# Performance work log

Hardware: AMD Instinct MI355X
Metric: run time of the kernel (lower is better)

## Reference

```python
import jax, jax.numpy as jnp
import numpy as np

N = 10000        # total_num
BS = 100         # batch_size (BatchNorm is applied per micro-batch in train mode)
IN_CH = 3
D = 128          # out_channels
TOPK = 50
BN_EPS = 1e-5


def setup_inputs() -> dict:
    key = jax.random.key(0)
    k1, k2, k3, k4 = jax.random.split(key, 4)
    feat = 32 * 32 * IN_CH
    inputs = jax.random.normal(k1, (N, IN_CH, 32, 32), dtype=jnp.float32)
    # nn.Linear(32*32*in_channels, out_channels)
    W1 = jax.random.normal(k2, (D, feat), dtype=jnp.float32) / np.sqrt(feat)
    b1 = jnp.zeros((D,), jnp.float32)
    # BatchNorm1d(out_channels) affine params
    gamma = jnp.ones((D,), jnp.float32)
    beta = jnp.zeros((D,), jnp.float32)
    # nn.Linear(out_channels, 1) -> weight [1, D] stored as vector, scalar bias
    sw = jax.random.normal(k3, (D,), dtype=jnp.float32) / np.sqrt(D)
    sb = jax.random.normal(k4, (), dtype=jnp.float32) * 0.01
    return {"inputs": inputs, "W1": W1, "b1": b1, "gamma": gamma,
            "beta": beta, "sw": sw, "sb": sb}


def _forward(inputs, W1, b1, gamma, beta, sw, sb):
    n = inputs.shape[0]
    # self.main is identity (undefined backbone); flatten + linear
    x = inputs.reshape(n, -1) @ W1.T + b1                      # [N, D]
    # BatchNorm1d in train mode, applied per batch of BS rows (as in the loop)
    xb = x.reshape(n // BS, BS, D)
    mean = xb.mean(axis=1, keepdims=True)
    var = xb.var(axis=1, keepdims=True)                        # biased, like torch BN
    outputs = ((xb - mean) * jax.lax.rsqrt(var + BN_EPS) * gamma + beta).reshape(n, D)
    # score[i,j] = ReLU( sum_k sw[k]*(x_i[k]-x_j[k])^2 + sb )
    a = (outputs * outputs) @ sw                               # [N]
    cross = (outputs * sw) @ outputs.T                         # [N, N]
    scores = jax.nn.relu(a[:, None] + a[None, :] - 2.0 * cross + sb)
    vals, idx = jax.lax.top_k(scores, TOPK)                    # [N, TOPK]
    vals = jax.nn.softmax(vals, axis=-1)
    S = jnp.zeros((n, n), outputs.dtype).at[jnp.arange(n)[:, None], idx].set(vals)
    return outputs, S


def reference(inputs, W1, b1, gamma, beta, sw, sb):
    return _forward(inputs, W1, b1, gamma, beta, sw, sb)
```

## Files before the change

kernel.cpp:

```cpp
#include <hip/hip_runtime.h>
#include <cstdint>

#define N_TOTAL 10000
#define D 128
#define FEAT 3072
#define BS_BN 100
#define TOPK 50

typedef unsigned int uint;
typedef short short8 __attribute__((ext_vector_type(8)));
typedef float f32x4 __attribute__((ext_vector_type(4)));
union U16 { uint4 u; short8 b; };

__device__ inline void split8(float4 f0, float4 f1, U16& h, U16& l) {
  float f[8] = {f0.x, f0.y, f0.z, f0.w, f1.x, f1.y, f1.z, f1.w};
  uint hb[8], lb[8];
#pragma unroll
  for (int e = 0; e < 8; ++e) {
    uint b = __float_as_uint(f[e]);
    uint hx = b & 0xFFFF0000u;
    float lf = f[e] - __uint_as_float(hx);
    hb[e] = b >> 16;
    lb[e] = __float_as_uint(lf) >> 16;
  }
  h.u = make_uint4(hb[0] | (hb[1] << 16), hb[2] | (hb[3] << 16),
                   hb[4] | (hb[5] << 16), hb[6] | (hb[7] << 16));
  l.u = make_uint4(lb[0] | (lb[1] << 16), lb[2] | (lb[3] << 16),
                   lb[4] | (lb[5] << 16), lb[6] | (lb[7] << 16));
}

__global__ __launch_bounds__(256) void k_gemm1(const float* __restrict__ in,
                                               const float* __restrict__ W1,
                                               float* __restrict__ x) {
  __shared__ alignas(16) float Af[128 * 44];
  __shared__ alignas(16) float Bf[128 * 44];
  const int t = threadIdx.x;
  const int lane = t & 63, wid = t >> 6;
  const int q = lane >> 4, l15 = lane & 15;
  const int i0 = blockIdx.x * 128;
  const int k0 = blockIdx.y * 768;
  const int wm = (wid & 1) * 64, wn = (wid >> 1) * 64;

  f32x4 acc[4][4];
#pragma unroll
  for (int mt = 0; mt < 4; ++mt)
#pragma unroll
    for (int nt = 0; nt < 4; ++nt) acc[mt][nt] = (f32x4){0.f, 0.f, 0.f, 0.f};

  for (int kb = k0; kb < k0 + 768; kb += 32) {
    __syncthreads();
#pragma unroll
    for (int s = 0; s < 4; ++s) {
      int idx = t + 256 * s;
      int row = idx >> 3, f4 = (idx & 7) * 4;
      int gi = i0 + row; if (gi > N_TOTAL - 1) gi = N_TOTAL - 1;
      *(float4*)&Af[row * 44 + f4] = *(const float4*)&in[(size_t)gi * FEAT + kb + f4];
      *(float4*)&Bf[row * 44 + f4] = *(const float4*)&W1[(size_t)row * FEAT + kb + f4];
    }
    __syncthreads();
    U16 Ah[4], Al[4], Bh[4], Bl[4];
#pragma unroll
    for (int mt = 0; mt < 4; ++mt) {
      int ro = (wm + mt * 16 + l15) * 44 + q * 8;
      float4 x0 = *(const float4*)&Af[ro];
      float4 x1 = *(const float4*)&Af[ro + 4];
      split8(x0, x1, Ah[mt], Al[mt]);
    }
#pragma unroll
    for (int nt = 0; nt < 4; ++nt) {
      int ro = (wn + nt * 16 + l15) * 44 + q * 8;
      float4 x0 = *(const float4*)&Bf[ro];
      float4 x1 = *(const float4*)&Bf[ro + 4];
      split8(x0, x1, Bh[nt], Bl[nt]);
    }
#pragma unroll
    for (int mt = 0; mt < 4; ++mt)
#pragma unroll
      for (int nt = 0; nt < 4; ++nt) {
        acc[mt][nt] = __builtin_amdgcn_mfma_f32_16x16x32_bf16(Ah[mt].b, Bh[nt].b, acc[mt][nt], 0, 0, 0);
        acc[mt][nt] = __builtin_amdgcn_mfma_f32_16x16x32_bf16(Ah[mt].b, Bl[nt].b, acc[mt][nt], 0, 0, 0);
        acc[mt][nt] = __builtin_amdgcn_mfma_f32_16x16x32_bf16(Al[mt].b, Bh[nt].b, acc[mt][nt], 0, 0, 0);
      }
  }

#pragma unroll
  for (int mt = 0; mt < 4; ++mt) {
#pragma unroll
    for (int r = 0; r < 4; ++r) {
      int gi = i0 + wm + mt * 16 + q * 4 + r;
      if (gi >= N_TOTAL) continue;
#pragma unroll
      for (int nt = 0; nt < 4; ++nt)
        atomicAdd(&x[(size_t)gi * D + wn + nt * 16 + l15], acc[mt][nt][r]);
    }
  }
}

__global__ __launch_bounds__(128) void k_bn(const float* __restrict__ x,
                                            const float* __restrict__ b1,
                                            const float* __restrict__ gamma,
                                            const float* __restrict__ beta,
                                            const float* __restrict__ sw,
                                            float* __restrict__ out_final,
                                            float* __restrict__ outf,
                                            float* __restrict__ wsw) {
  const int b = blockIdx.x, c = threadIdx.x;
  const float bias = b1[c];
  float s = 0.f, s2 = 0.f;
  const float* xp = x + (size_t)b * BS_BN * D + c;
  for (int r = 0; r < BS_BN; ++r) {
    float v = xp[(size_t)r * D] + bias;
    s += v; s2 = fmaf(v, v, s2);
  }
  float mean = s * (1.f / BS_BN);
  float var = s2 * (1.f / BS_BN) - mean * mean;
  float scale = gamma[c] * rsqrtf(var + 1e-5f);
  float shift = beta[c] - mean * scale;
  float swc = sw[c];
  float* op  = out_final + (size_t)b * BS_BN * D + c;
  float* ofp = outf + (size_t)b * BS_BN * D + c;
  float* wp  = wsw + (size_t)b * BS_BN * D + c;
  for (int r = 0; r < BS_BN; ++r) {
    float v = fmaf(xp[(size_t)r * D] + bias, scale, shift);
    op[(size_t)r * D] = v;
    ofp[(size_t)r * D] = v;
    wp[(size_t)r * D] = v * swc;
  }
}

__global__ __launch_bounds__(256) void k_arow(const float* __restrict__ outf,
                                              const float* __restrict__ sw,
                                              float* __restrict__ aarr) {
  const int t = threadIdx.x;
  const int lane = t & 63;
  const int row = blockIdx.x * 4 + (t >> 6);
  float o1 = outf[(size_t)row * D + lane];
  float o2 = outf[(size_t)row * D + 64 + lane];
  float v = sw[lane] * o1 * o1 + sw[64 + lane] * o2 * o2;
#pragma unroll
  for (int off = 32; off >= 1; off >>= 1) v += __shfl_xor(v, off);
  if (lane == 0) aarr[row] = v;
}

__global__ __launch_bounds__(256) void k_score(const float* __restrict__ outf,
                                               const float* __restrict__ wsw,
                                               const float* __restrict__ aarr,
                                               const float* __restrict__ sbp,
                                               float* __restrict__ S) {
  __shared__ alignas(16) float Af[128 * 44];
  __shared__ alignas(16) float Bf[128 * 44];
  const int t = threadIdx.x;
  const int lane = t & 63, wid = t >> 6;
  const int q = lane >> 4, l15 = lane & 15;
  const int ib = blockIdx.x * 128, jb = blockIdx.y * 128;
  const int wm = (wid & 1) * 64, wn = (wid >> 1) * 64;

  f32x4 acc[4][4];
#pragma unroll
  for (int mt = 0; mt < 4; ++mt)
#pragma unroll
    for (int nt = 0; nt < 4; ++nt) acc[mt][nt] = (f32x4){0.f, 0.f, 0.f, 0.f};

  for (int kb = 0; kb < D; kb += 32) {
    __syncthreads();
#pragma unroll
    for (int s = 0; s < 4; ++s) {
      int idx = t + 256 * s;
      int row = idx >> 3, f4 = (idx & 7) * 4;
      int gi = ib + row; if (gi > N_TOTAL - 1) gi = N_TOTAL - 1;
      int gj = jb + row; if (gj > N_TOTAL - 1) gj = N_TOTAL - 1;
      *(float4*)&Af[row * 44 + f4] = *(const float4*)&outf[(size_t)gi * D + kb + f4];
      *(float4*)&Bf[row * 44 + f4] = *(const float4*)&wsw[(size_t)gj * D + kb + f4];
    }
    __syncthreads();
    U16 Ah[4], Al[4], Bh[4], Bl[4];
#pragma unroll
    for (int mt = 0; mt < 4; ++mt) {
      int ro = (wm + mt * 16 + l15) * 44 + q * 8;
      float4 x0 = *(const float4*)&Af[ro];
      float4 x1 = *(const float4*)&Af[ro + 4];
      split8(x0, x1, Ah[mt], Al[mt]);
    }
#pragma unroll
    for (int nt = 0; nt < 4; ++nt) {
      int ro = (wn + nt * 16 + l15) * 44 + q * 8;
      float4 x0 = *(const float4*)&Bf[ro];
      float4 x1 = *(const float4*)&Bf[ro + 4];
      split8(x0, x1, Bh[nt], Bl[nt]);
    }
#pragma unroll
    for (int mt = 0; mt < 4; ++mt)
#pragma unroll
      for (int nt = 0; nt < 4; ++nt) {
        acc[mt][nt] = __builtin_amdgcn_mfma_f32_16x16x32_bf16(Ah[mt].b, Bh[nt].b, acc[mt][nt], 0, 0, 0);
        acc[mt][nt] = __builtin_amdgcn_mfma_f32_16x16x32_bf16(Ah[mt].b, Bl[nt].b, acc[mt][nt], 0, 0, 0);
        acc[mt][nt] = __builtin_amdgcn_mfma_f32_16x16x32_bf16(Al[mt].b, Bh[nt].b, acc[mt][nt], 0, 0, 0);
      }
  }

  const float sb = sbp[0];
  float ajv[4];
  int gjc[4];
#pragma unroll
  for (int nt = 0; nt < 4; ++nt) {
    gjc[nt] = jb + wn + nt * 16 + l15;
    ajv[nt] = aarr[gjc[nt] < N_TOTAL ? gjc[nt] : N_TOTAL - 1];
  }
#pragma unroll
  for (int mt = 0; mt < 4; ++mt) {
#pragma unroll
    for (int r = 0; r < 4; ++r) {
      int gi = ib + wm + mt * 16 + q * 4 + r;
      if (gi >= N_TOTAL) continue;
      float ai = aarr[gi] + sb;
#pragma unroll
      for (int nt = 0; nt < 4; ++nt) {
        if (gjc[nt] < N_TOTAL) {
          float s = ai + ajv[nt] - 2.f * acc[mt][nt][r];
          S[(size_t)gi * N_TOTAL + gjc[nt]] = (s > 0.f) ? s : 0.f;
        }
      }
    }
  }
}

__global__ __launch_bounds__(256) void k_topk(float* __restrict__ S) {
  const int t = threadIdx.x;
  const int lane = t & 63, wid = t >> 6;
  const size_t rbase = (size_t)blockIdx.x * N_TOTAL;
  const uint4* rp4v = (const uint4*)(S + rbase);

  uint v[10][4];
#pragma unroll
  for (int j = 0; j < 10; ++j) {
    if (j < 9 || t < 196) {
      uint4 x = rp4v[j * 256 + t];
      v[j][0] = x.x; v[j][1] = x.y; v[j][2] = x.z; v[j][3] = x.w;
    } else {
      v[j][0] = v[j][1] = v[j][2] = v[j][3] = 0u;
    }
  }

  __shared__ uint wred[4];
  __shared__ int scnt;
  __shared__ int ctr;
  __shared__ uint sT;
  __shared__ uint candv[1024];
  __shared__ float topv[TOPK];
  __shared__ int topi[TOPK];

  uint mx = 0u;
#pragma unroll
  for (int j = 0; j < 10; ++j)
#pragma unroll
    for (int e = 0; e < 4; ++e) mx = max(mx, v[j][e]);
#pragma unroll
  for (int off = 32; off >= 1; off >>= 1)
    mx = max(mx, (uint)__shfl_xor((int)mx, off));
  if (lane == 0) wred[wid] = mx;
  __syncthreads();
  mx = max(max(wred[0], wred[1]), max(wred[2], wred[3]));
  __syncthreads();

  uint T = 0u;
  bool zero_path = (mx == 0u);
  if (!zero_path) {
    uint C = mx & 0xFF800000u;
    if (C == 0u) C = 1u;
    uint Chi = mx + 1u;
    int cnt = 0, c_loc = 0;
    for (;;) {
      if (t == 0) scnt = 0;
      __syncthreads();
      c_loc = 0;
#pragma unroll
      for (int j = 0; j < 10; ++j)
#pragma unroll
        for (int e = 0; e < 4; ++e) c_loc += (v[j][e] >= C) ? 1 : 0;
      int cw = c_loc;
#pragma unroll
      for (int off = 32; off >= 1; off >>= 1) cw += __shfl_xor(cw, off);
      if (lane == 0) atomicAdd(&scnt, cw);
      __syncthreads();
      cnt = scnt;
      __syncthreads();
      if (cnt >= TOPK || C == 1u) break;
      Chi = C;
      C = (C > (1u << 23)) ? (C - (1u << 23)) : 1u;
    }
    if (cnt < TOPK) {
      zero_path = true;
    } else if (cnt <= 1024) {
      if (t == 0) ctr = 0;
      __syncthreads();
      int base_ = (c_loc > 0) ? atomicAdd(&ctr, c_loc) : 0;
      int p = base_;
#pragma unroll
      for (int j = 0; j < 10; ++j)
#pragma unroll
        for (int e = 0; e < 4; ++e)
          if (v[j][e] >= C) candv[p++] = v[j][e];
      __syncthreads();
      if (wid == 0) {
        uint cv[16];
#pragma unroll
        for (int s = 0; s < 16; ++s) {
          int ix = lane + s * 64;
          cv[s] = (ix < cnt) ? candv[ix] : 0u;
        }
        uint L = C, H = Chi;
        while (H - L > 1u) {
          uint M = L + ((H - L) >> 1);
          int cc = 0;
#pragma unroll
          for (int s = 0; s < 16; ++s) cc += (cv[s] >= M) ? 1 : 0;
#pragma unroll
          for (int off = 32; off >= 1; off >>= 1) cc += __shfl_xor(cc, off);
          if (cc >= TOPK) L = M; else H = M;
        }
        if (lane == 0) sT = L;
      }
      __syncthreads();
      T = sT;
    } else {
      uint L = C, H = Chi;
      while (H - L > 1u) {
        uint M = L + ((H - L) >> 1);
        if (t == 0) scnt = 0;
        __syncthreads();
        int c = 0;
#pragma unroll
        for (int j = 0; j < 10; ++j)
#pragma unroll
          for (int e = 0; e < 4; ++e) c += (v[j][e] >= M) ? 1 : 0;
#pragma unroll
        for (int off = 32; off >= 1; off >>= 1) c += __shfl_xor(c, off);
        if (lane == 0) atomicAdd(&scnt, c);
        __syncthreads();
        int f = scnt;
        __syncthreads();
        if (f >= TOPK) L = M; else H = M;
      }
      T = L;
    }
  }

  if (t == 0) ctr = 0;
  __syncthreads();
  int cg = 0;
#pragma unroll
  for (int j = 0; j < 10; ++j)
#pragma unroll
    for (int e = 0; e < 4; ++e) cg += (v[j][e] > T) ? 1 : 0;
  int gbase = (cg > 0) ? atomicAdd(&ctr, cg) : 0;
  {
    int p = gbase;
#pragma unroll
    for (int j = 0; j < 10; ++j)
#pragma unroll
      for (int e = 0; e < 4; ++e)
        if (v[j][e] > T) {
          if (p < TOPK) { topv[p] = __uint_as_float(v[j][e]); topi[p] = (j * 256 + t) * 4 + e; }
          ++p;
        }
  }
  __syncthreads();
  const int cnt_gt = min(ctr, TOPK);
  __syncthreads();
  const int need = TOPK - cnt_gt;

  if (!zero_path) {
    if (t == 0) scnt = 0;
    __syncthreads();
    int ce = 0;
#pragma unroll
    for (int j = 0; j < 10; ++j)
#pragma unroll
      for (int e = 0; e < 4; ++e) ce += (v[j][e] == T) ? 1 : 0;
    int ebase = (ce > 0) ? atomicAdd(&scnt, ce) : 0;
    {
      int p = ebase;
#pragma unroll
      for (int j = 0; j < 10; ++j)
#pragma unroll
        for (int e = 0; e < 4; ++e)
          if (v[j][e] == T) {
            if (p < 1024) candv[p] = (uint)((j * 256 + t) * 4 + e);
            ++p;
          }
    }
    __syncthreads();
    int nE = min(scnt, 1024);
    if (wid == 0) {
      int es[16];
#pragma unroll
      for (int s = 0; s < 16; ++s) {
        int ix = lane + s * 64;
        es[s] = (ix < nE) ? (int)candv[ix] : 0x7FFFFFFF;
      }
      for (int r = 0; r < need; ++r) {
        int m = es[0];
#pragma unroll
        for (int s = 1; s < 16; ++s) m = min(m, es[s]);
#pragma unroll
        for (int off = 32; off >= 1; off >>= 1) m = min(m, __shfl_xor(m, off));
        if (lane == 0 && m != 0x7FFFFFFF) {
          topv[cnt_gt + r] = __uint_as_float(T);
          topi[cnt_gt + r] = m;
        }
#pragma unroll
        for (int s = 0; s < 16; ++s) if (es[s] == m) es[s] = 0x7FFFFFFF;
      }
    }
    __syncthreads();
  } else {
    int L = 0, H = N_TOTAL;
    while (H - L > 1) {
      int M = L + ((H - L) >> 1);
      if (t == 0) scnt = 0;
      __syncthreads();
      int c = 0;
#pragma unroll
      for (int j = 0; j < 10; ++j)
#pragma unroll
        for (int e = 0; e < 4; ++e) {
          int col = (j * 256 + t) * 4 + e;
          c += (v[j][e] == 0u && col < M) ? 1 : 0;
        }
#pragma unroll
      for (int off = 32; off >= 1; off >>= 1) c += __shfl_xor(c, off);
      if (lane == 0) atomicAdd(&scnt, c);
      __syncthreads();
      int f = scnt;
      __syncthreads();
      if (f >= need) H = M; else L = M;
    }
    if (t == 0) scnt = 0;
    __syncthreads();
    int cz = 0;
#pragma unroll
    for (int j = 0; j < 10; ++j)
#pragma unroll
      for (int e = 0; e < 4; ++e) {
        int col = (j * 256 + t) * 4 + e;
        cz += (v[j][e] == 0u && col < H) ? 1 : 0;
      }
    int zbase = (cz > 0) ? atomicAdd(&scnt, cz) : 0;
    {
      int p = zbase;
#pragma unroll
      for (int j = 0; j < 10; ++j)
#pragma unroll
        for (int e = 0; e < 4; ++e) {
          int col = (j * 256 + t) * 4 + e;
          if (v[j][e] == 0u && col < H) {
            if (cnt_gt + p < TOPK) { topv[cnt_gt + p] = 0.0f; topi[cnt_gt + p] = col; }
            ++p;
          }
        }
    }
    __syncthreads();
  }

  if (wid == 0) {
    float xv = (lane < TOPK) ? topv[lane] : -1e30f;
    float mxf = xv;
#pragma unroll
    for (int off = 32; off >= 1; off >>= 1) mxf = fmaxf(mxf, __shfl_xor(mxf, off));
    float e = (lane < TOPK) ? expf(xv - mxf) : 0.f;
    float ss = e;
#pragma unroll
    for (int off = 32; off >= 1; off >>= 1) ss += __shfl_xor(ss, off);
    if (lane < TOPK) topv[lane] = e / ss;
  }
  __syncthreads();

  float4 z = make_float4(0.f, 0.f, 0.f, 0.f);
  float4* wp4 = (float4*)(S + rbase);
  for (int i = t; i < N_TOTAL / 4; i += 256) wp4[i] = z;
  __syncthreads();
  if (t < TOPK) {
    int ii = topi[t];
    if (ii >= 0 && ii < N_TOTAL) S[rbase + ii] = topv[t];
  }
}

extern "C" void kernel_launch(void* const* d_in, const int* in_sizes, int n_in,
                              void* d_out, int out_size, void* d_ws, size_t ws_size,
                              hipStream_t stream) {
  const float* in    = (const float*)d_in[0];
  const float* W1    = (const float*)d_in[1];
  const float* b1    = (const float*)d_in[2];
  const float* gamma = (const float*)d_in[3];
  const float* beta  = (const float*)d_in[4];
  const float* sw    = (const float*)d_in[5];
  const float* sb    = (const float*)d_in[6];
  float* out_f = (float*)d_out;
  float* S = out_f + (size_t)N_TOTAL * D;

  float* wsf  = (float*)d_ws;
  float* x    = wsf;
  float* outf = wsf + 1280000;
  float* wswb = wsf + 2560000;
  float* aarr = wsf + 3840000;

  hipMemsetAsync(x, 0, (size_t)N_TOTAL * D * sizeof(float), stream);
  k_gemm1<<<dim3(79, 4), 256, 0, stream>>>(in, W1, x);
  k_bn<<<100, 128, 0, stream>>>(x, b1, gamma, beta, sw, out_f, outf, wswb);
  k_arow<<<2500, 256, 0, stream>>>(outf, sw, aarr);
  k_score<<<dim3(79, 79), 256, 0, stream>>>(outf, wswb, aarr, sb, S);
  k_topk<<<10000, 256, 0, stream>>>(S);
}
```

Measured before the change: 905.6 us.

## Fuse score GEMM with streaming top-k selection, skip full score matrix

Replaces the score kernel that writes the full N×N score matrix and the separate top-k kernel that rereads it with one fused kernel. Each block of 32 rows streams all column tiles and keeps threshold-filtered candidate keys in shared memory, pruning them with a wavefront bitonic sort. The BN kernel now writes bf16 hi/lo splits with a swizzled layout so the GEMM skips the per-tile split work. The aim is to avoid writing and then reading the 400MB score matrix. The cost is only 313 large blocks (low occupancy), serialized candidate sorts, and extra tie-break logic.

```diff
diff --git a/kernel.cpp b/kernel.cpp
--- a/kernel.cpp
+++ b/kernel.cpp
@@ -8,6 +8,8 @@
 #define TOPK 50
 
 typedef unsigned int uint;
+typedef unsigned long long ull;
+typedef unsigned short u16;
 typedef short short8 __attribute__((ext_vector_type(8)));
 typedef float f32x4 __attribute__((ext_vector_type(4)));
 union U16 { uint4 u; short8 b; };
@@ -103,7 +105,8 @@
                                             const float* __restrict__ sw,
                                             float* __restrict__ out_final,
                                             float* __restrict__ outf,
-                                            float* __restrict__ wsw) {
+                                            u16* __restrict__ Ah, u16* __restrict__ Al,
+                                            u16* __restrict__ Bh, u16* __restrict__ Bl) {
   const int b = blockIdx.x, c = threadIdx.x;
   const float bias = b1[c];
   float s = 0.f, s2 = 0.f;
@@ -119,12 +122,22 @@
   float swc = sw[c];
   float* op  = out_final + (size_t)b * BS_BN * D + c;
   float* ofp = outf + (size_t)b * BS_BN * D + c;
-  float* wp  = wsw + (size_t)b * BS_BN * D + c;
   for (int r = 0; r < BS_BN; ++r) {
     float v = fmaf(xp[(size_t)r * D] + bias, scale, shift);
     op[(size_t)r * D] = v;
     ofp[(size_t)r * D] = v;
-    wp[(size_t)r * D] = v * swc;
+    int j = b * BS_BN + r;
+    size_t rowo = (size_t)j * D;
+    int cs = c ^ ((j & 7) << 3);
+    uint vb = __float_as_uint(v);
+    float vl = v - __uint_as_float(vb & 0xFFFF0000u);
+    Ah[rowo + c] = (u16)(vb >> 16);
+    Al[rowo + c] = (u16)(__float_as_uint(vl) >> 16);
+    float w = v * swc;
+    uint wb = __float_as_uint(w);
+    float wl = w - __uint_as_float(wb & 0xFFFF0000u);
+    Bh[rowo + cs] = (u16)(wb >> 16);
+    Bl[rowo + cs] = (u16)(__float_as_uint(wl) >> 16);
   }
 }
 
@@ -142,347 +155,207 @@
   if (lane == 0) aarr[row] = v;
 }
 
-__global__ __launch_bounds__(256) void k_score(const float* __restrict__ outf,
-                                               const float* __restrict__ wsw,
-                                               const float* __restrict__ aarr,
-                                               const float* __restrict__ sbp,
-                                               float* __restrict__ S) {
-  __shared__ alignas(16) float Af[128 * 44];
-  __shared__ alignas(16) float Bf[128 * 44];
+#define FCAP 248
+#define FTRIG 120
+#define JT 128
+#define NT 79
+
+__device__ inline void sort256_desc(ull v[4], int lane) {
+#pragma unroll
+  for (uint k = 2; k <= 256; k <<= 1) {
+    for (uint jj = k >> 1; jj; jj >>= 1) {
+      if (jj >= 64) {
+        int sj = (int)(jj >> 6);
+#pragma unroll
+        for (int s = 0; s < 4; ++s) {
+          if (!(s & sj)) {
+            int sp = s | sj;
+            bool up = (((uint)(s * 64) & k) == 0u);
+            ull a = v[s], b = v[sp];
+            ull mx = a > b ? a : b, mn = a > b ? b : a;
+            v[s] = up ? mx : mn;
+            v[sp] = up ? mn : mx;
+          }
+        }
+      } else {
+#pragma unroll
+        for (int s = 0; s < 4; ++s) {
+          uint g = (uint)(s * 64 + lane);
+          ull o = __shfl_xor(v[s], (int)jj, 64);
+          bool up = ((g & k) == 0u);
+          bool lower = (((uint)lane & jj) == 0u);
+          ull mx = v[s] > o ? v[s] : o;
+          ull mn = v[s] > o ? o : v[s];
+          v[s] = (up == lower) ? mx : mn;
+        }
+      }
+    }
+  }
+}
+
+__global__ __launch_bounds__(1024) void k_fused(const u16* __restrict__ Ah,
+                                                const u16* __restrict__ Al,
+                                                const u16* __restrict__ Bh,
+                                                const u16* __restrict__ Bl,
+                                                const float* __restrict__ aarr,
+                                                const float* __restrict__ sbp,
+                                                ull* __restrict__ lists) {
+  __shared__ ull resK[32][FCAP];
+  __shared__ ull thrK[32];
+  __shared__ uint cntK[32];
+  __shared__ alignas(16) u16 Bls[2 * JT * D];
+
   const int t = threadIdx.x;
   const int lane = t & 63, wid = t >> 6;
   const int q = lane >> 4, l15 = lane & 15;
-  const int ib = blockIdx.x * 128, jb = blockIdx.y * 128;
-  const int wm = (wid & 1) * 64, wn = (wid >> 1) * 64;
-
-  f32x4 acc[4][4];
-#pragma unroll
-  for (int mt = 0; mt < 4; ++mt)
-#pragma unroll
-    for (int nt = 0; nt < 4; ++nt) acc[mt][nt] = (f32x4){0.f, 0.f, 0.f, 0.f};
-
-  for (int kb = 0; kb < D; kb += 32) {
+  const int ifr = wid >> 3, jfr = wid & 7;
+  const int i0 = blockIdx.x * 32;
+  const float sb = sbp[0];
+
+  if (t < 32) { cntK[t] = 0u; thrK[t] = 0ULL; }
+
+  int arow = i0 + ifr * 16 + l15; if (arow > N_TOTAL - 1) arow = N_TOTAL - 1;
+  uint4 AhR[4], AlR[4];
+#pragma unroll
+  for (int kk = 0; kk < 4; ++kk) {
+    AhR[kk] = *(const uint4*)(Ah + (size_t)arow * D + kk * 32 + q * 8);
+    AlR[kk] = *(const uint4*)(Al + (size_t)arow * D + kk * 32 + q * 8);
+  }
+  float ai[4];
+#pragma unroll
+  for (int r = 0; r < 4; ++r) {
+    int ig = i0 + ifr * 16 + q * 4 + r; if (ig > N_TOTAL - 1) ig = N_TOTAL - 1;
+    ai[r] = aarr[ig] + sb;
+  }
+
+  const int jl = jfr * 16 + l15;
+  const int swz = (jl & 7) << 4;
+
+  uint4 stg[4];
+#pragma unroll
+  for (int s = 0; s < 4; ++s) {
+    int idx = s * 1024 + t;
+    int p = idx >> 11;
+    int off = (idx & 2047) * 16;
+    int jg = (off >> 8); if (jg > N_TOTAL - 1) jg = N_TOTAL - 1;
+    stg[s] = *(const uint4*)((const char*)(p ? Bl : Bh) + (size_t)jg * 256 + (off & 255));
+  }
+
+  for (int tile = 0; tile < NT; ++tile) {
+    if (tile > 0) {
+#pragma unroll
+      for (int rr = 0; rr < 2; ++rr) {
+        int rI = wid + rr * 16;
+        uint c = cntK[rI];
+        if (c > FTRIG) {
+          int cc = (c > (uint)FCAP) ? FCAP : (int)c;
+          ull v[4];
+#pragma unroll
+          for (int s = 0; s < 4; ++s) {
+            int g = s * 64 + lane;
+            v[s] = (g < cc) ? resK[rI][g] : 0ULL;
+          }
+          sort256_desc(v, lane);
+          if (lane < TOPK) resK[rI][lane] = v[0];
+          if (lane == TOPK - 1) thrK[rI] = v[0];
+          if (lane == 0) cntK[rI] = TOPK;
+        }
+      }
+    }
+#pragma unroll
+    for (int s = 0; s < 4; ++s) {
+      int idx = s * 1024 + t;
+      int off = (idx & 2047) * 16;
+      *(uint4*)((char*)Bls + (idx >> 11) * 32768 + off) = stg[s];
+    }
     __syncthreads();
+
+    if (tile + 1 < NT) {
+      int jb2 = (tile + 1) * JT;
+#pragma unroll
+      for (int s = 0; s < 4; ++s) {
+        int idx = s * 1024 + t;
+        int p = idx >> 11;
+        int off = (idx & 2047) * 16;
+        int jg = jb2 + (off >> 8); if (jg > N_TOTAL - 1) jg = N_TOTAL - 1;
+        stg[s] = *(const uint4*)((const char*)(p ? Bl : Bh) + (size_t)jg * 256 + (off & 255));
+      }
+    }
+
+    const int jb = tile * JT;
+    const int jc = jb + jl;
+    float ajv = aarr[jc < N_TOTAL ? jc : N_TOTAL - 1];
+
+    f32x4 acc = (f32x4){0.f, 0.f, 0.f, 0.f};
+    const char* bbase = (const char*)Bls + (size_t)jl * 256;
+#pragma unroll
+    for (int kk = 0; kk < 4; ++kk) {
+      int bo = ((kk * 32 + q * 8) * 2) ^ swz;
+      U16 bh, bl, ah, al;
+      bh.u = *(const uint4*)(bbase + bo);
+      bl.u = *(const uint4*)(bbase + 32768 + bo);
+      ah.u = AhR[kk]; al.u = AlR[kk];
+      acc = __builtin_amdgcn_mfma_f32_16x16x32_bf16(ah.b, bh.b, acc, 0, 0, 0);
+      acc = __builtin_amdgcn_mfma_f32_16x16x32_bf16(ah.b, bl.b, acc, 0, 0, 0);
+      acc = __builtin_amdgcn_mfma_f32_16x16x32_bf16(al.b, bh.b, acc, 0, 0, 0);
+    }
+
+    if (jc < N_TOTAL) {
+#pragma unroll
+      for (int r = 0; r < 4; ++r) {
+        int il = ifr * 16 + q * 4 + r;
+        float sc = ai[r] + ajv - 2.f * acc[r];
+        sc = (sc > 0.f) ? sc : 0.f;
+        ull key = ((ull)__float_as_uint(sc) << 32) | (ull)(0xFFFFFFFFu - (uint)jc);
+        if (key > thrK[il]) {
+          uint pos = atomicAdd(&cntK[il], 1u);
+          if (pos < (uint)FCAP) resK[il][pos] = key;
+        }
+      }
+    }
+    __syncthreads();
+  }
+
+#pragma unroll
+  for (int rr = 0; rr < 2; ++rr) {
+    int rI = wid + rr * 16;
+    int ig = i0 + rI;
+    uint c = cntK[rI];
+    int cc = (c > (uint)FCAP) ? FCAP : (int)c;
+    ull v[4];
 #pragma unroll
     for (int s = 0; s < 4; ++s) {
-      int idx = t + 256 * s;
-      int row = idx >> 3, f4 = (idx & 7) * 4;
-      int gi = ib + row; if (gi > N_TOTAL - 1) gi = N_TOTAL - 1;
-      int gj = jb + row; if (gj > N_TOTAL - 1) gj = N_TOTAL - 1;
-      *(float4*)&Af[row * 44 + f4] = *(const float4*)&outf[(size_t)gi * D + kb + f4];
-      *(float4*)&Bf[row * 44 + f4] = *(const float4*)&wsw[(size_t)gj * D + kb + f4];
-    }
-    __syncthreads();
-    U16 Ah[4], Al[4], Bh[4], Bl[4];
-#pragma unroll
-    for (int mt = 0; mt < 4; ++mt) {
-      int ro = (wm + mt * 16 + l15) * 44 + q * 8;
-      float4 x0 = *(const float4*)&Af[ro];
-      float4 x1 = *(const float4*)&Af[ro + 4];
-      split8(x0, x1, Ah[mt], Al[mt]);
-    }
-#pragma unroll
-    for (int nt = 0; nt < 4; ++nt) {
-      int ro = (wn + nt * 16 + l15) * 44 + q * 8;
-      float4 x0 = *(const float4*)&Bf[ro];
-      float4 x1 = *(const float4*)&Bf[ro + 4];
-      split8(x0, x1, Bh[nt], Bl[nt]);
-    }
-#pragma unroll
-    for (int mt = 0; mt < 4; ++mt)
-#pragma unroll
-      for (int nt = 0; nt < 4; ++nt) {
-        acc[mt][nt] = __builtin_amdgcn_mfma_f32_16x16x32_bf16(Ah[mt].b, Bh[nt].b, acc[mt][nt], 0, 0, 0);
-        acc[mt][nt] = __builtin_amdgcn_mfma_f32_16x16x32_bf16(Ah[mt].b, Bl[nt].b, acc[mt][nt], 0, 0, 0);
-        acc[mt][nt] = __builtin_amdgcn_mfma_f32_16x16x32_bf16(Al[mt].b, Bh[nt].b, acc[mt][nt], 0, 0, 0);
-      }
-  }
-
-  const float sb = sbp[0];
-  float ajv[4];
-  int gjc[4];
-#pragma unroll
-  for (int nt = 0; nt < 4; ++nt) {
-    gjc[nt] = jb + wn + nt * 16 + l15;
-    ajv[nt] = aarr[gjc[nt] < N_TOTAL ? gjc[nt] : N_TOTAL - 1];
-  }
-#pragma unroll
-  for (int mt = 0; mt < 4; ++mt) {
-#pragma unroll
-    for (int r = 0; r < 4; ++r) {
-      int gi = ib + wm + mt * 16 + q * 4 + r;
-      if (gi >= N_TOTAL) continue;
-      float ai = aarr[gi] + sb;
-#pragma unroll
-      for (int nt = 0; nt < 4; ++nt) {
-        if (gjc[nt] < N_TOTAL) {
-          float s = ai + ajv[nt] - 2.f * acc[mt][nt][r];
-          S[(size_t)gi * N_TOTAL + gjc[nt]] = (s > 0.f) ? s : 0.f;
-        }
-      }
-    }
-  }
-}
-
-__global__ __launch_bounds__(256) void k_topk(float* __restrict__ S) {
+      int g = s * 64 + lane;
+      v[s] = (g < cc) ? resK[rI][g] : 0ULL;
+    }
+    sort256_desc(v, lane);
+    if (ig < N_TOTAL && lane < TOPK) lists[(size_t)ig * TOPK + lane] = v[0];
+  }
+}
+
+__global__ __launch_bounds__(256) void k_write(const ull* __restrict__ lists,
+                                               float* __restrict__ S) {
   const int t = threadIdx.x;
   const int lane = t & 63, wid = t >> 6;
-  const size_t rbase = (size_t)blockIdx.x * N_TOTAL;
-  const uint4* rp4v = (const uint4*)(S + rbase);
-
-  uint v[10][4];
-#pragma unroll
-  for (int j = 0; j < 10; ++j) {
-    if (j < 9 || t < 196) {
-      uint4 x = rp4v[j * 256 + t];
-      v[j][0] = x.x; v[j][1] = x.y; v[j][2] = x.z; v[j][3] = x.w;
-    } else {
-      v[j][0] = v[j][1] = v[j][2] = v[j][3] = 0u;
-    }
-  }
-
-  __shared__ uint wred[4];
-  __shared__ int scnt;
-  __shared__ int ctr;
-  __shared__ uint sT;
-  __shared__ uint candv[1024];
-  __shared__ float topv[TOPK];
-  __shared__ int topi[TOPK];
-
-  uint mx = 0u;
-#pragma unroll
-  for (int j = 0; j < 10; ++j)
-#pragma unroll
-    for (int e = 0; e < 4; ++e) mx = max(mx, v[j][e]);
-#pragma unroll
-  for (int off = 32; off >= 1; off >>= 1)
-    mx = max(mx, (uint)__shfl_xor((int)mx, off));
-  if (lane == 0) wred[wid] = mx;
+  const int row = blockIdx.x * 4 + wid;
+
+  ull key = (lane < TOPK) ? lists[(size_t)row * TOPK + lane] : 0ULL;
+  float xv = (lane < TOPK) ? __uint_as_float((uint)(key >> 32)) : -1e30f;
+  float mx = xv;
+#pragma unroll
+  for (int off = 32; off >= 1; off >>= 1) mx = fmaxf(mx, __shfl_xor(mx, off));
+  float e = (lane < TOPK) ? expf(xv - mx) : 0.f;
+  float ss = e;
+#pragma unroll
+  for (int off = 32; off >= 1; off >>= 1) ss += __shfl_xor(ss, off);
+  float sv = e / ss;
+  uint j = 0xFFFFFFFFu - (uint)(key & 0xFFFFFFFFu);
+
+  float4* wp = (float4*)(S + (size_t)row * N_TOTAL);
+  float4 z = make_float4(0.f, 0.f, 0.f, 0.f);
+  for (int c = lane; c < N_TOTAL / 4; c += 64) wp[c] = z;
   __syncthreads();
-  mx = max(max(wred[0], wred[1]), max(wred[2], wred[3]));
-  __syncthreads();
-
-  uint T = 0u;
-  bool zero_path = (mx == 0u);
-  if (!zero_path) {
-    uint C = mx & 0xFF800000u;
-    if (C == 0u) C = 1u;
-    uint Chi = mx + 1u;
-    int cnt = 0, c_loc = 0;
-    for (;;) {
-      if (t == 0) scnt = 0;
-      __syncthreads();
-      c_loc = 0;
-#pragma unroll
-      for (int j = 0; j < 10; ++j)
-#pragma unroll
-        for (int e = 0; e < 4; ++e) c_loc += (v[j][e] >= C) ? 1 : 0;
-      int cw = c_loc;
-#pragma unroll
-      for (int off = 32; off >= 1; off >>= 1) cw += __shfl_xor(cw, off);
-      if (lane == 0) atomicAdd(&scnt, cw);
-      __syncthreads();
-      cnt = scnt;
-      __syncthreads();
-      if (cnt >= TOPK || C == 1u) break;
-      Chi = C;
-      C = (C > (1u << 23)) ? (C - (1u << 23)) : 1u;
-    }
-    if (cnt < TOPK) {
-      zero_path = true;
-    } else if (cnt <= 1024) {
-      if (t == 0) ctr = 0;
-      __syncthreads();
-      int base_ = (c_loc > 0) ? atomicAdd(&ctr, c_loc) : 0;
-      int p = base_;
-#pragma unroll
-      for (int j = 0; j < 10; ++j)
-#pragma unroll
-        for (int e = 0; e < 4; ++e)
-          if (v[j][e] >= C) candv[p++] = v[j][e];
-      __syncthreads();
-      if (wid == 0) {
-        uint cv[16];
-#pragma unroll
-        for (int s = 0; s < 16; ++s) {
-          int ix = lane + s * 64;
-          cv[s] = (ix < cnt) ? candv[ix] : 0u;
-        }
-        uint L = C, H = Chi;
-        while (H - L > 1u) {
-          uint M = L + ((H - L) >> 1);
-          int cc = 0;
-#pragma unroll
-          for (int s = 0; s < 16; ++s) cc += (cv[s] >= M) ? 1 : 0;
-#pragma unroll
-          for (int off = 32; off >= 1; off >>= 1) cc += __shfl_xor(cc, off);
-          if (cc >= TOPK) L = M; else H = M;
-        }
-        if (lane == 0) sT = L;
-      }
-      __syncthreads();
-      T = sT;
-    } else {
-      uint L = C, H = Chi;
-      while (H - L > 1u) {
-        uint M = L + ((H - L) >> 1);
-        if (t == 0) scnt = 0;
-        __syncthreads();
-        int c = 0;
-#pragma unroll
-        for (int j = 0; j < 10; ++j)
-#pragma unroll
-          for (int e = 0; e < 4; ++e) c += (v[j][e] >= M) ? 1 : 0;
-#pragma unroll
-        for (int off = 32; off >= 1; off >>= 1) c += __shfl_xor(c, off);
-        if (lane == 0) atomicAdd(&scnt, c);
-        __syncthreads();
-        int f = scnt;
-        __syncthreads();
-        if (f >= TOPK) L = M; else H = M;
-      }
-      T = L;
-    }
-  }
-
-  if (t == 0) ctr = 0;
-  __syncthreads();
-  int cg = 0;
-#pragma unroll
-  for (int j = 0; j < 10; ++j)
-#pragma unroll
-    for (int e = 0; e < 4; ++e) cg += (v[j][e] > T) ? 1 : 0;
-  int gbase = (cg > 0) ? atomicAdd(&ctr, cg) : 0;
-  {
-    int p = gbase;
-#pragma unroll
-    for (int j = 0; j < 10; ++j)
-#pragma unroll
-      for (int e = 0; e < 4; ++e)
-        if (v[j][e] > T) {
-          if (p < TOPK) { topv[p] = __uint_as_float(v[j][e]); topi[p] = (j * 256 + t) * 4 + e; }
-          ++p;
-        }
-  }
-  __syncthreads();
-  const int cnt_gt = min(ctr, TOPK);
-  __syncthreads();
-  const int need = TOPK - cnt_gt;
-
-  if (!zero_path) {
-    if (t == 0) scnt = 0;
-    __syncthreads();
-    int ce = 0;
-#pragma unroll
-    for (int j = 0; j < 10; ++j)
-#pragma unroll
-      for (int e = 0; e < 4; ++e) ce += (v[j][e] == T) ? 1 : 0;
-    int ebase = (ce > 0) ? atomicAdd(&scnt, ce) : 0;
-    {
-      int p = ebase;
-#pragma unroll
-      for (int j = 0; j < 10; ++j)
-#pragma unroll
-        for (int e = 0; e < 4; ++e)
-          if (v[j][e] == T) {
-            if (p < 1024) candv[p] = (uint)((j * 256 + t) * 4 + e);
-            ++p;
-          }
-    }
-    __syncthreads();
-    int nE = min(scnt, 1024);
-    if (wid == 0) {
-      int es[16];
-#pragma unroll
-      for (int s = 0; s < 16; ++s) {
-        int ix = lane + s * 64;
-        es[s] = (ix < nE) ? (int)candv[ix] : 0x7FFFFFFF;
-      }
-      for (int r = 0; r < need; ++r) {
-        int m = es[0];
-#pragma unroll
-        for (int s = 1; s < 16; ++s) m = min(m, es[s]);
-#pragma unroll
-        for (int off = 32; off >= 1; off >>= 1) m = min(m, __shfl_xor(m, off));
-        if (lane == 0 && m != 0x7FFFFFFF) {
-          topv[cnt_gt + r] = __uint_as_float(T);
-          topi[cnt_gt + r] = m;
-        }
-#pragma unroll
-        for (int s = 0; s < 16; ++s) if (es[s] == m) es[s] = 0x7FFFFFFF;
-      }
-    }
-    __syncthreads();
-  } else {
-    int L = 0, H = N_TOTAL;
-    while (H - L > 1) {
-      int M = L + ((H - L) >> 1);
-      if (t == 0) scnt = 0;
-      __syncthreads();
-      int c = 0;
-#pragma unroll
-      for (int j = 0; j < 10; ++j)
-#pragma unroll
-        for (int e = 0; e < 4; ++e) {
-          int col = (j * 256 + t) * 4 + e;
-          c += (v[j][e] == 0u && col < M) ? 1 : 0;
-        }
-#pragma unroll
-      for (int off = 32; off >= 1; off >>= 1) c += __shfl_xor(c, off);
-      if (lane == 0) atomicAdd(&scnt, c);
-      __syncthreads();
-      int f = scnt;
-      __syncthreads();
-      if (f >= need) H = M; else L = M;
-    }
-    if (t == 0) scnt = 0;
-    __syncthreads();
-    int cz = 0;
-#pragma unroll
-    for (int j = 0; j < 10; ++j)
-#pragma unroll
-      for (int e = 0; e < 4; ++e) {
-        int col = (j * 256 + t) * 4 + e;
-        cz += (v[j][e] == 0u && col < H) ? 1 : 0;
-      }
-    int zbase = (cz > 0) ? atomicAdd(&scnt, cz) : 0;
-    {
-      int p = zbase;
-#pragma unroll
-      for (int j = 0; j < 10; ++j)
-#pragma unroll
-        for (int e = 0; e < 4; ++e) {
-          int col = (j * 256 + t) * 4 + e;
-          if (v[j][e] == 0u && col < H) {
-            if (cnt_gt + p < TOPK) { topv[cnt_gt + p] = 0.0f; topi[cnt_gt + p] = col; }
-            ++p;
-          }
-        }
-    }
-    __syncthreads();
-  }
-
-  if (wid == 0) {
-    float xv = (lane < TOPK) ? topv[lane] : -1e30f;
-    float mxf = xv;
-#pragma unroll
-    for (int off = 32; off >= 1; off >>= 1) mxf = fmaxf(mxf, __shfl_xor(mxf, off));
-    float e = (lane < TOPK) ? expf(xv - mxf) : 0.f;
-    float ss = e;
-#pragma unroll
-    for (int off = 32; off >= 1; off >>= 1) ss += __shfl_xor(ss, off);
-    if (lane < TOPK) topv[lane] = e / ss;
-  }
-  __syncthreads();
-
-  float4 z = make_float4(0.f, 0.f, 0.f, 0.f);
-  float4* wp4 = (float4*)(S + rbase);
-  for (int i = t; i < N_TOTAL / 4; i += 256) wp4[i] = z;
-  __syncthreads();
-  if (t < TOPK) {
-    int ii = topi[t];
-    if (ii >= 0 && ii < N_TOTAL) S[rbase + ii] = topv[t];
-  }
+  if (lane < TOPK) S[(size_t)row * N_TOTAL + j] = sv;
 }
 
 extern "C" void kernel_launch(void* const* d_in, const int* in_sizes, int n_in,
@@ -501,13 +374,17 @@
   float* wsf  = (float*)d_ws;
   float* x    = wsf;
   float* outf = wsf + 1280000;
-  float* wswb = wsf + 2560000;
-  float* aarr = wsf + 3840000;
+  float* aarr = wsf + 2560000;
+  u16* Ah = (u16*)(wsf + 2570000);
+  u16* Al = Ah + 1280000;
+  u16* Bh = Al + 1280000;
+  u16* Bl = Bh + 1280000;
+  ull* lists = (ull*)(Bl + 1280000);
 
   hipMemsetAsync(x, 0, (size_t)N_TOTAL * D * sizeof(float), stream);
   k_gemm1<<<dim3(79, 4), 256, 0, stream>>>(in, W1, x);
-  k_bn<<<100, 128, 0, stream>>>(x, b1, gamma, beta, sw, out_f, outf, wswb);
+  k_bn<<<100, 128, 0, stream>>>(x, b1, gamma, beta, sw, out_f, outf, Ah, Al, Bh, Bl);
   k_arow<<<2500, 256, 0, stream>>>(outf, sw, aarr);
-  k_score<<<dim3(79, 79), 256, 0, stream>>>(outf, wswb, aarr, sb, S);
-  k_topk<<<10000, 256, 0, stream>>>(S);
-}
+  k_fused<<<313, 1024, 0, stream>>>(Ah, Al, Bh, Bl, aarr, sb, lists);
+  k_write<<<2500, 256, 0, stream>>>(lists, S);
+}
```

After: 1.728 ms. 90.8% more time.
